# Optimization experiments

Measured on AMD Instinct MI355X. Metric: run time of the kernel, lower is better.

## Reference

```python
import jax, jax.numpy as jnp
import numpy as np

K = 3
K2 = K * K
EPS = 1e-5


def conv2d(x, w, stride=1, pad=1):
    return jax.lax.conv_general_dilated(
        x, w, (stride, stride), [(pad, pad), (pad, pad)],
        dimension_numbers=("NCHW", "OIHW", "NCHW"))


def bilinear_sample(x, py, px):
    """x: [B,C,H,W]; py,px: [B,Ho,Wo,K2] float sample coords.
    Zero padding outside bounds (torchvision deform_conv2d semantics).
    Returns [B,C,Ho,Wo,K2]."""
    B, C, H, W = x.shape
    Ho, Wo = py.shape[1], py.shape[2]
    y0 = jnp.floor(py)
    x0 = jnp.floor(px)
    wy1 = py - y0
    wx1 = px - x0
    x_flat = x.reshape(B, C, H * W)

    def gather(yi, xi):
        valid = (yi >= 0) & (yi < H) & (xi >= 0) & (xi < W)
        yc = jnp.clip(yi, 0, H - 1).astype(jnp.int32)
        xc = jnp.clip(xi, 0, W - 1).astype(jnp.int32)
        idx = (yc * W + xc).reshape(B, 1, -1)          # [B,1,N]
        v = jnp.take_along_axis(x_flat, idx, axis=2)   # [B,C,N]
        return v * valid.reshape(B, 1, -1).astype(x.dtype)

    w00 = ((1 - wy1) * (1 - wx1)).reshape(B, 1, -1)
    w01 = ((1 - wy1) * wx1).reshape(B, 1, -1)
    w10 = (wy1 * (1 - wx1)).reshape(B, 1, -1)
    w11 = (wy1 * wx1).reshape(B, 1, -1)
    val = (w00 * gather(y0, x0) + w01 * gather(y0, x0 + 1)
           + w10 * gather(y0 + 1, x0) + w11 * gather(y0 + 1, x0 + 1))
    return val.reshape(B, C, Ho, Wo, K2)


def deform_conv_bn_relu(x, d, offset_w, conv_w, gamma, beta):
    # offset branch: 3x3 conv on d, clamp to [-1,1]
    offset = jnp.clip(conv2d(d, offset_w, 1, 1), -1.0, 1.0)  # [B,2*K2,H,W]
    B, Cin, H, W = x.shape
    Cout = conv_w.shape[0]
    off = offset.reshape(B, K2, 2, H, W)
    dy = off[:, :, 0].transpose(0, 2, 3, 1)  # [B,H,W,K2]
    dx = off[:, :, 1].transpose(0, 2, 3, 1)
    kh = (jnp.arange(K2) // K).astype(jnp.float32)
    kw = (jnp.arange(K2) % K).astype(jnp.float32)
    # sample coords: out pixel + kernel tap - padding + learned offset
    py = (jnp.arange(H, dtype=jnp.float32)[None, :, None, None] - 1.0
          + kh[None, None, None, :] + dy)
    px = (jnp.arange(W, dtype=jnp.float32)[None, None, :, None] - 1.0
          + kw[None, None, None, :] + dx)
    sampled = bilinear_sample(x, py, px)  # [B,Cin,H,W,K2]
    out = jnp.einsum('bchwk,ock->bohw', sampled,
                     conv_w.reshape(Cout, Cin, K2))
    # BatchNorm2d (training forward: biased batch stats) + ReLU
    mean = out.mean(axis=(0, 2, 3))
    var = out.var(axis=(0, 2, 3))
    inv = gamma / jnp.sqrt(var + EPS)
    out = (out - mean[None, :, None, None]) * inv[None, :, None, None] \
        + beta[None, :, None, None]
    out = jax.nn.relu(out)
    return out, offset


def setup_inputs() -> dict:
    key = jax.random.key(0)
    k1, k2, k3, k4 = jax.random.split(key, 4)
    B, C, H, W = 4, 64, 160, 160
    Cout, offC = 64, 64
    x = jax.random.normal(k1, (B, C, H, W), dtype=jnp.float32)
    d = jax.random.normal(k2, (B, offC, H, W), dtype=jnp.float32)
    # torch zero-inits offset_conv; use small random weights so the
    # bilinear gather path is actually exercised with fractional offsets
    offset_w = jax.random.normal(k3, (2 * K2, offC, K, K), dtype=jnp.float32) * 0.01
    conv_w = jax.random.normal(k4, (Cout, C, K, K), dtype=jnp.float32) * (1.0 / np.sqrt(C * K2))
    gamma = jnp.ones((Cout,), dtype=jnp.float32)
    beta = jnp.zeros((Cout,), dtype=jnp.float32)
    return {"x": x, "d": d, "offset_w": offset_w, "conv_w": conv_w,
            "gamma": gamma, "beta": beta}


def reference(x, d, offset_w, conv_w, gamma, beta):
    return deform_conv_bn_relu(x, d, offset_w, conv_w, gamma, beta)
```

## Files before the change

### kernel.cpp

```cpp
#include <hip/hip_runtime.h>
#include <hip/hip_bf16.h>

#define BB 4
#define HH 160
#define WW 160
#define HWD (HH * WW)
#define OUT_ELEMS (BB * 64 * HWD)
#define OFF_ELEMS (BB * 18 * HWD)
#define EPSBN 1e-5f
#define CHSTRIDE (8 * HWD)
#define NSLOT 256

typedef __attribute__((ext_vector_type(8))) short bf16x8;
typedef __attribute__((ext_vector_type(4))) float f32x4;

__device__ inline unsigned pack2bf(float a, float b) {
  __hip_bfloat162 h2 = __float22bfloat162_rn(float2{a, b});
  unsigned u;
  __builtin_memcpy(&u, &h2, 4);
  return u;
}
__device__ inline unsigned short bf16bits(float a) {
  __hip_bfloat16 h = __float2bfloat16(a);
  unsigned short u;
  __builtin_memcpy(&u, &h, 2);
  return u;
}

__device__ inline void tile_map(int blk, int& b, int& ty0, int& tx0) {
  int t = (blk & 7) * 200 + (blk >> 3);
  b = t / 400;
  int r = t % 400;
  ty0 = (r / 10) * 4;
  tx0 = (r % 10) * 16;
}

__global__ void prep_kernel(const float* __restrict__ cw,
                            const float* __restrict__ ow,
                            unsigned short* __restrict__ Bp,
                            unsigned short* __restrict__ B2p,
                            float* __restrict__ part) {
  int i = blockIdx.x * 256 + threadIdx.x;
  if (i < 32768) part[i] = 0.f;
  if (i < 49152) {
    int j = i & 7, l = (i >> 3) & 63, rest = i >> 9;
    int ki = rest % 24, nt = rest / 24;
    int kp = ki * 32 + ((l >> 4) << 3) + j;
    int chunk = kp / 96, kq = kp % 96;
    int t = kq >> 3, c = kq & 7;
    int n = nt * 16 + (l & 15);
    float v = (t < 9) ? cw[n * 576 + (chunk * 8 + c) * 9 + t] : 0.f;
    Bp[i] = bf16bits(v);
  }
  if (i < 24576) {
    int j = i & 7, l = (i >> 3) & 63, rest = i >> 9;
    int ki = rest % 24, nt = rest / 24;
    int kp = ki * 32 + ((l >> 4) << 3) + j;
    int chunk = kp / 96, kq = kp % 96;
    int t = kq >> 3, c = kq & 7;
    int n = nt * 16 + (l & 15);
    float v = (t < 9 && n < 18) ? ow[n * 576 + (chunk * 8 + c) * 9 + t] : 0.f;
    B2p[i] = bf16bits(v);
  }
}

__global__ __launch_bounds__(256, 4) void fused_kernel(
    const float* __restrict__ x, const float* __restrict__ d,
    const bf16x8* __restrict__ Bp, const bf16x8* __restrict__ B2p,
    float* __restrict__ out, float* __restrict__ off_out,
    float* __restrict__ part) {
  int b, ty0, tx0;
  tile_map(blockIdx.x, b, ty0, tx0);
  const int tid = threadIdx.x;
  const int wv = tid >> 6, lane = tid & 63;
  const int lo = lane >> 4, li = lane & 15;
  const int px = li, py = wv;
  const int h = ty0 + py, w = tx0 + px;

  __shared__ float patch[189 * 12];
  __shared__ bf16x8 Af[768];
  __shared__ float offs_s[64 * 18];

  int goffx[6], laddrx[6];
  bool gokx[6];
#pragma unroll
  for (int i = 0; i < 6; ++i) {
    int l = tid + i * 256;
    int c = l / 189, rc = l % 189, r = rc / 21, col = rc % 21;
    int gy = ty0 - 2 + r, gx = tx0 - 2 + col;
    gokx[i] = (l < 1512) && gy >= 0 && gy < HH && gx >= 0 && gx < WW;
    goffx[i] = ((b * 64 + c) * HH + gy) * WW + gx;
    laddrx[i] = rc * 12 + c;
  }

  f32x4 acc0{0.f, 0.f, 0.f, 0.f}, acc1{0.f, 0.f, 0.f, 0.f};
  const int ntA = wv >> 1, mh = wv & 1;
  {
    int poff[3];
    bool tre[3];
#pragma unroll
    for (int kk = 0; kk < 3; ++kk) {
      int t = kk * 4 + lo;
      tre[kk] = (t < 9);
      poff[kk] = tre[kk] ? ((py + t / 3) * 18 + px + t % 3) : 0;
    }

    int goff[4], laddr[4];
    bool gok[4];
#pragma unroll
    for (int i = 0; i < 4; ++i) {
      int l = tid + i * 256;
      int c = l / 108, rc = l % 108, r = rc / 18, col = rc % 18;
      int gy = ty0 - 1 + r, gx = tx0 - 1 + col;
      gok[i] = (l < 864) && gy >= 0 && gy < HH && gx < WW && gx >= 0;
      goff[i] = ((b * 64 + c) * HH + gy) * WW + gx;
      laddr[i] = rc * 12 + c;
    }
    float g[4];
#pragma unroll
    for (int i = 0; i < 4; ++i) g[i] = gok[i] ? d[goff[i]] : 0.f;

    for (int chunk = 0; chunk < 8; ++chunk) {
      bf16x8 bw0 = B2p[((ntA * 24 + chunk * 3 + 0) << 6) + lane];
      bf16x8 bw1 = B2p[((ntA * 24 + chunk * 3 + 1) << 6) + lane];
      bf16x8 bw2 = B2p[((ntA * 24 + chunk * 3 + 2) << 6) + lane];
#pragma unroll
      for (int i = 0; i < 4; ++i) {
        int l = tid + i * 256;
        if (l < 864) patch[laddr[i]] = g[i];
      }
      __syncthreads();
      int nco = ((chunk < 7) ? (chunk + 1) : 7) * CHSTRIDE;
#pragma unroll
      for (int i = 0; i < 4; ++i) g[i] = gok[i] ? d[goff[i] + nco] : 0.f;
#pragma unroll
      for (int kk = 0; kk < 3; ++kk) {
        union { bf16x8 v; unsigned u[4]; } a;
        if (tre[kk]) {
          const float* q = patch + poff[kk] * 12;
          float4 c0 = *(const float4*)(q);
          float4 c1 = *(const float4*)(q + 4);
          a.u[0] = pack2bf(c0.x, c0.y);
          a.u[1] = pack2bf(c0.z, c0.w);
          a.u[2] = pack2bf(c1.x, c1.y);
          a.u[3] = pack2bf(c1.z, c1.w);
        } else {
          a.u[0] = a.u[1] = a.u[2] = a.u[3] = 0u;
        }
        Af[((wv * 3 + kk) << 6) + lane] = a.v;
      }
      __syncthreads();
#pragma unroll
      for (int kk = 0; kk < 3; ++kk) {
        bf16x8 bw = (kk == 0) ? bw0 : (kk == 1) ? bw1 : bw2;
        acc0 = __builtin_amdgcn_mfma_f32_16x16x32_bf16(
            Af[(((mh * 2) * 3 + kk) << 6) + lane], bw, acc0, 0, 0, 0);
        acc1 = __builtin_amdgcn_mfma_f32_16x16x32_bf16(
            Af[(((mh * 2 + 1) * 3 + kk) << 6) + lane], bw, acc1, 0, 0, 0);
      }
    }
  }

  float gv[6];
#pragma unroll
  for (int i = 0; i < 6; ++i) gv[i] = gokx[i] ? x[goffx[i]] : 0.f;

  {
    const int n = ntA * 16 + li;
    if (n < 18) {
#pragma unroll
      for (int f = 0; f < 2; ++f) {
        int mf = mh * 2 + f;
        f32x4 a = f ? acc1 : acc0;
        float* po =
            off_out + ((b * 18 + n) * HH + ty0 + mf) * WW + tx0 + lo * 4;
        float4 v;
        v.x = fminf(1.f, fmaxf(-1.f, a[0]));
        v.y = fminf(1.f, fmaxf(-1.f, a[1]));
        v.z = fminf(1.f, fmaxf(-1.f, a[2]));
        v.w = fminf(1.f, fmaxf(-1.f, a[3]));
        *(float4*)po = v;
        int pix = mf * 16 + lo * 4;
        offs_s[(pix + 0) * 18 + n] = v.x;
        offs_s[(pix + 1) * 18 + n] = v.y;
        offs_s[(pix + 2) * 18 + n] = v.z;
        offs_s[(pix + 3) * 18 + n] = v.w;
      }
    }
  }
  __syncthreads();

  int bs[3];
  float W00[3], W01[3], W10[3], W11[3];
  bool tre[3];
#pragma unroll
  for (int kk = 0; kk < 3; ++kk) {
    int t = kk * 4 + lo;
    tre[kk] = (t < 9);
    if (tre[kk]) {
      float dy = offs_s[(py * 16 + px) * 18 + 2 * t];
      float dx = offs_s[(py * 16 + px) * 18 + 2 * t + 1];
      float pyf = (float)(h - 1 + t / 3) + dy;
      float pxf = (float)(w - 1 + t % 3) + dx;
      float y0 = floorf(pyf), x0 = floorf(pxf);
      float wy = pyf - y0, wx = pxf - x0;
      bs[kk] = ((int)y0 - (ty0 - 2)) * 21 + ((int)x0 - (tx0 - 2));
      W00[kk] = (1.f - wy) * (1.f - wx);
      W01[kk] = (1.f - wy) * wx;
      W10[kk] = wy * (1.f - wx);
      W11[kk] = wy * wx;
    } else {
      bs[kk] = 0;
      W00[kk] = W01[kk] = W10[kk] = W11[kk] = 0.f;
    }
  }

  f32x4 acc[4];
#pragma unroll
  for (int i = 0; i < 4; ++i) acc[i] = f32x4{0.f, 0.f, 0.f, 0.f};
  const int nt = wv;

  for (int chunk = 0; chunk < 8; ++chunk) {
    bf16x8 bw0 = Bp[((nt * 24 + chunk * 3 + 0) << 6) + lane];
    bf16x8 bw1 = Bp[((nt * 24 + chunk * 3 + 1) << 6) + lane];
    bf16x8 bw2 = Bp[((nt * 24 + chunk * 3 + 2) << 6) + lane];
#pragma unroll
    for (int i = 0; i < 6; ++i) {
      int l = tid + i * 256;
      if (l < 1512) patch[laddrx[i]] = gv[i];
    }
    __syncthreads();
    int nco = ((chunk < 7) ? (chunk + 1) : 7) * CHSTRIDE;
#pragma unroll
    for (int i = 0; i < 6; ++i) gv[i] = gokx[i] ? x[goffx[i] + nco] : 0.f;
#pragma unroll
    for (int kk = 0; kk < 3; ++kk) {
      union { bf16x8 v; unsigned u[4]; } a;
      if (tre[kk]) {
        const float* q = patch + bs[kk] * 12;
        float4 p00a = *(const float4*)(q);
        float4 p00b = *(const float4*)(q + 4);
        float4 p01a = *(const float4*)(q + 12);
        float4 p01b = *(const float4*)(q + 16);
        float4 p10a = *(const float4*)(q + 252);
        float4 p10b = *(const float4*)(q + 256);
        float4 p11a = *(const float4*)(q + 264);
        float4 p11b = *(const float4*)(q + 268);
        float w0 = W00[kk], w1 = W01[kk], w2 = W10[kk], w3 = W11[kk];
        float v0 = fmaf(w3, p11a.x, fmaf(w2, p10a.x, fmaf(w1, p01a.x, w0 * p00a.x)));
        float v1 = fmaf(w3, p11a.y, fmaf(w2, p10a.y, fmaf(w1, p01a.y, w0 * p00a.y)));
        float v2 = fmaf(w3, p11a.z, fmaf(w2, p10a.z, fmaf(w1, p01a.z, w0 * p00a.z)));
        float v3 = fmaf(w3, p11a.w, fmaf(w2, p10a.w, fmaf(w1, p01a.w, w0 * p00a.w)));
        float v4 = fmaf(w3, p11b.x, fmaf(w2, p10b.x, fmaf(w1, p01b.x, w0 * p00b.x)));
        float v5 = fmaf(w3, p11b.y, fmaf(w2, p10b.y, fmaf(w1, p01b.y, w0 * p00b.y)));
        float v6 = fmaf(w3, p11b.z, fmaf(w2, p10b.z, fmaf(w1, p01b.z, w0 * p00b.z)));
        float v7 = fmaf(w3, p11b.w, fmaf(w2, p10b.w, fmaf(w1, p01b.w, w0 * p00b.w)));
        a.u[0] = pack2bf(v0, v1);
        a.u[1] = pack2bf(v2, v3);
        a.u[2] = pack2bf(v4, v5);
        a.u[3] = pack2bf(v6, v7);
      } else {
        a.u[0] = a.u[1] = a.u[2] = a.u[3] = 0u;
      }
      Af[((wv * 3 + kk) << 6) + lane] = a.v;
    }
    __syncthreads();
#pragma unroll
    for (int kk = 0; kk < 3; ++kk) {
      bf16x8 bw = (kk == 0) ? bw0 : (kk == 1) ? bw1 : bw2;
#pragma unroll
      for (int mf = 0; mf < 4; ++mf)
        acc[mf] = __builtin_amdgcn_mfma_f32_16x16x32_bf16(
            Af[((mf * 3 + kk) << 6) + lane], bw, acc[mf], 0, 0, 0);
    }
  }
  const int n = nt * 16 + li;
  float s = 0.f, s2 = 0.f;
#pragma unroll
  for (int mf = 0; mf < 4; ++mf) {
    float* po = out + ((b * 64 + n) * HH + ty0 + mf) * WW + tx0 + lo * 4;
    *(float4*)po = make_float4(acc[mf][0], acc[mf][1], acc[mf][2], acc[mf][3]);
#pragma unroll
    for (int r = 0; r < 4; ++r) {
      float v = acc[mf][r];
      s += v;
      s2 = fmaf(v, v, s2);
    }
  }
  s += __shfl_xor(s, 16);  s += __shfl_xor(s, 32);
  s2 += __shfl_xor(s2, 16); s2 += __shfl_xor(s2, 32);
  if (lo == 0) {
    int slot = blockIdx.x & (NSLOT - 1);
    atomicAdd(&part[n * NSLOT + slot], s);
    atomicAdd(&part[(64 + n) * NSLOT + slot], s2);
  }
}

__global__ __launch_bounds__(256) void reduce_kernel(
    const float* __restrict__ part, double* __restrict__ sums) {
  const int j = blockIdx.x;
  __shared__ double sh[256];
  sh[threadIdx.x] = (double)part[j * NSLOT + threadIdx.x];
  __syncthreads();
  for (int t = 128; t > 0; t >>= 1) {
    if (threadIdx.x < t) sh[threadIdx.x] += sh[threadIdx.x + t];
    __syncthreads();
  }
  if (threadIdx.x == 0) sums[j] = sh[0];
}

__global__ __launch_bounds__(256) void bnapply_kernel(
    float* __restrict__ out, const double* __restrict__ sums,
    const float* __restrict__ gamma, const float* __restrict__ beta) {
  const int i = blockIdx.x * 256 + threadIdx.x;
  if (i >= OUT_ELEMS / 4) return;
  const int o = (i / (HWD / 4)) & 63;
  const float n_inv = 1.0f / (float)(BB * HWD);
  float mean = (float)sums[o] * n_inv;
  float var = (float)sums[64 + o] * n_inv - mean * mean;
  float inv = gamma[o] * rsqrtf(var + EPSBN);
  float bt = beta[o];
  float4 v = ((float4*)out)[i];
  v.x = fmaxf(0.f, (v.x - mean) * inv + bt);
  v.y = fmaxf(0.f, (v.y - mean) * inv + bt);
  v.z = fmaxf(0.f, (v.z - mean) * inv + bt);
  v.w = fmaxf(0.f, (v.w - mean) * inv + bt);
  ((float4*)out)[i] = v;
}

extern "C" void kernel_launch(void* const* d_in, const int* in_sizes, int n_in,
                              void* d_out, int out_size, void* d_ws, size_t ws_size,
                              hipStream_t stream) {
  const float* x = (const float*)d_in[0];
  const float* d = (const float*)d_in[1];
  const float* ow = (const float*)d_in[2];
  const float* cw = (const float*)d_in[3];
  const float* gamma = (const float*)d_in[4];
  const float* beta = (const float*)d_in[5];

  float* out = (float*)d_out;
  float* off_out = out + OUT_ELEMS;

  double* sums = (double*)d_ws;
  unsigned short* Bp = (unsigned short*)((char*)d_ws + 1024);
  unsigned short* B2p = Bp + 49152;
  float* part = (float*)(B2p + 24576);

  prep_kernel<<<192, 256, 0, stream>>>(cw, ow, Bp, B2p, part);

  fused_kernel<<<1600, 256, 0, stream>>>(x, d, (const bf16x8*)Bp,
                                         (const bf16x8*)B2p, out, off_out,
                                         part);

  reduce_kernel<<<128, 256, 0, stream>>>(part, sums);
  bnapply_kernel<<<(OUT_ELEMS / 4 + 255) / 256, 256, 0, stream>>>(
      out, sums, gamma, beta);
}
```

Measured before the change: 161.7 us.

## Keep MFMA A-fragments in registers and double-buffer the input patch

Each wave now feeds its own sampled pixel-row fragments straight into MFMA as the A operand and loops over all output-channel tiles, so the Af shared-memory staging buffer and the second __syncthreads per channel chunk are gone. The input patch is double-buffered so the next chunk's store does not race with reads of the current one. In exchange each wave loads all the weight fragments per chunk, which raises register pressure and global/L2 weight traffic, and the epilogue now issues four times as many atomics per lane.

```diff
diff --git a/kernel.cpp b/kernel.cpp
--- a/kernel.cpp
+++ b/kernel.cpp
@@ -6,7 +6,6 @@
 #define WW 160
 #define HWD (HH * WW)
 #define OUT_ELEMS (BB * 64 * HWD)
-#define OFF_ELEMS (BB * 18 * HWD)
 #define EPSBN 1e-5f
 #define CHSTRIDE (8 * HWD)
 #define NSLOT 256
@@ -77,8 +76,7 @@
   const int px = li, py = wv;
   const int h = ty0 + py, w = tx0 + px;
 
-  __shared__ float patch[189 * 12];
-  __shared__ bf16x8 Af[768];
+  __shared__ float patch[2][189 * 12];
   __shared__ float offs_s[64 * 18];
 
   int goffx[6], laddrx[6];
@@ -93,16 +91,17 @@
     laddrx[i] = rc * 12 + c;
   }
 
-  f32x4 acc0{0.f, 0.f, 0.f, 0.f}, acc1{0.f, 0.f, 0.f, 0.f};
-  const int ntA = wv >> 1, mh = wv & 1;
+  int cur = 0;
+
+  f32x4 po0{0.f, 0.f, 0.f, 0.f}, po1{0.f, 0.f, 0.f, 0.f};
   {
     int poff[3];
-    bool tre[3];
+    bool tre1[3];
 #pragma unroll
     for (int kk = 0; kk < 3; ++kk) {
       int t = kk * 4 + lo;
-      tre[kk] = (t < 9);
-      poff[kk] = tre[kk] ? ((py + t / 3) * 18 + px + t % 3) : 0;
+      tre1[kk] = (t < 9);
+      poff[kk] = tre1[kk] ? ((py + t / 3) * 18 + px + t % 3) : 0;
     }
 
     int goff[4], laddr[4];
@@ -112,7 +111,7 @@
       int l = tid + i * 256;
       int c = l / 108, rc = l % 108, r = rc / 18, col = rc % 18;
       int gy = ty0 - 1 + r, gx = tx0 - 1 + col;
-      gok[i] = (l < 864) && gy >= 0 && gy < HH && gx < WW && gx >= 0;
+      gok[i] = (l < 864) && gy >= 0 && gy < HH && gx >= 0 && gx < WW;
       goff[i] = ((b * 64 + c) * HH + gy) * WW + gx;
       laddr[i] = rc * 12 + c;
     }
@@ -121,43 +120,40 @@
     for (int i = 0; i < 4; ++i) g[i] = gok[i] ? d[goff[i]] : 0.f;
 
     for (int chunk = 0; chunk < 8; ++chunk) {
-      bf16x8 bw0 = B2p[((ntA * 24 + chunk * 3 + 0) << 6) + lane];
-      bf16x8 bw1 = B2p[((ntA * 24 + chunk * 3 + 1) << 6) + lane];
-      bf16x8 bw2 = B2p[((ntA * 24 + chunk * 3 + 2) << 6) + lane];
 #pragma unroll
       for (int i = 0; i < 4; ++i) {
         int l = tid + i * 256;
-        if (l < 864) patch[laddr[i]] = g[i];
+        if (l < 864) patch[cur][laddr[i]] = g[i];
       }
       __syncthreads();
       int nco = ((chunk < 7) ? (chunk + 1) : 7) * CHSTRIDE;
 #pragma unroll
       for (int i = 0; i < 4; ++i) g[i] = gok[i] ? d[goff[i] + nco] : 0.f;
+      const bf16x8* Bc = B2p + ((chunk * 3) << 6) + lane;
+      bf16x8 w00 = Bc[0], w01 = Bc[64], w02 = Bc[128];
+      bf16x8 w10 = Bc[1536], w11 = Bc[1600], w12 = Bc[1664];
+      union { bf16x8 v; unsigned u[4]; } a[3];
 #pragma unroll
       for (int kk = 0; kk < 3; ++kk) {
-        union { bf16x8 v; unsigned u[4]; } a;
-        if (tre[kk]) {
-          const float* q = patch + poff[kk] * 12;
+        if (tre1[kk]) {
+          const float* q = patch[cur] + poff[kk] * 12;
           float4 c0 = *(const float4*)(q);
           float4 c1 = *(const float4*)(q + 4);
-          a.u[0] = pack2bf(c0.x, c0.y);
-          a.u[1] = pack2bf(c0.z, c0.w);
-          a.u[2] = pack2bf(c1.x, c1.y);
-          a.u[3] = pack2bf(c1.z, c1.w);
+          a[kk].u[0] = pack2bf(c0.x, c0.y);
+          a[kk].u[1] = pack2bf(c0.z, c0.w);
+          a[kk].u[2] = pack2bf(c1.x, c1.y);
+          a[kk].u[3] = pack2bf(c1.z, c1.w);
         } else {
-          a.u[0] = a.u[1] = a.u[2] = a.u[3] = 0u;
+          a[kk].u[0] = a[kk].u[1] = a[kk].u[2] = a[kk].u[3] = 0u;
         }
-        Af[((wv * 3 + kk) << 6) + lane] = a.v;
       }
-      __syncthreads();
-#pragma unroll
-      for (int kk = 0; kk < 3; ++kk) {
-        bf16x8 bw = (kk == 0) ? bw0 : (kk == 1) ? bw1 : bw2;
-        acc0 = __builtin_amdgcn_mfma_f32_16x16x32_bf16(
-            Af[(((mh * 2) * 3 + kk) << 6) + lane], bw, acc0, 0, 0, 0);
-        acc1 = __builtin_amdgcn_mfma_f32_16x16x32_bf16(
-            Af[(((mh * 2 + 1) * 3 + kk) << 6) + lane], bw, acc1, 0, 0, 0);
-      }
+      po0 = __builtin_amdgcn_mfma_f32_16x16x32_bf16(a[0].v, w00, po0, 0, 0, 0);
+      po0 = __builtin_amdgcn_mfma_f32_16x16x32_bf16(a[1].v, w01, po0, 0, 0, 0);
+      po0 = __builtin_amdgcn_mfma_f32_16x16x32_bf16(a[2].v, w02, po0, 0, 0, 0);
+      po1 = __builtin_amdgcn_mfma_f32_16x16x32_bf16(a[0].v, w10, po1, 0, 0, 0);
+      po1 = __builtin_amdgcn_mfma_f32_16x16x32_bf16(a[1].v, w11, po1, 0, 0, 0);
+      po1 = __builtin_amdgcn_mfma_f32_16x16x32_bf16(a[2].v, w12, po1, 0, 0, 0);
+      cur ^= 1;
     }
   }
 
@@ -166,21 +162,19 @@
   for (int i = 0; i < 6; ++i) gv[i] = gokx[i] ? x[goffx[i]] : 0.f;
 
   {
-    const int n = ntA * 16 + li;
-    if (n < 18) {
-#pragma unroll
-      for (int f = 0; f < 2; ++f) {
-        int mf = mh * 2 + f;
-        f32x4 a = f ? acc1 : acc0;
-        float* po =
-            off_out + ((b * 18 + n) * HH + ty0 + mf) * WW + tx0 + lo * 4;
+    const int y = ty0 + wv;
+#pragma unroll
+    for (int nf = 0; nf < 2; ++nf) {
+      int n = nf * 16 + li;
+      if (n < 18) {
+        f32x4 aa = nf ? po1 : po0;
         float4 v;
-        v.x = fminf(1.f, fmaxf(-1.f, a[0]));
-        v.y = fminf(1.f, fmaxf(-1.f, a[1]));
-        v.z = fminf(1.f, fmaxf(-1.f, a[2]));
-        v.w = fminf(1.f, fmaxf(-1.f, a[3]));
-        *(float4*)po = v;
-        int pix = mf * 16 + lo * 4;
+        v.x = fminf(1.f, fmaxf(-1.f, aa[0]));
+        v.y = fminf(1.f, fmaxf(-1.f, aa[1]));
+        v.z = fminf(1.f, fmaxf(-1.f, aa[2]));
+        v.w = fminf(1.f, fmaxf(-1.f, aa[3]));
+        *(float4*)(off_out + ((b * 18 + n) * HH + y) * WW + tx0 + lo * 4) = v;
+        int pix = wv * 16 + lo * 4;
         offs_s[(pix + 0) * 18 + n] = v.x;
         offs_s[(pix + 1) * 18 + n] = v.y;
         offs_s[(pix + 2) * 18 + n] = v.z;
@@ -198,10 +192,9 @@
     int t = kk * 4 + lo;
     tre[kk] = (t < 9);
     if (tre[kk]) {
-      float dy = offs_s[(py * 16 + px) * 18 + 2 * t];
-      float dx = offs_s[(py * 16 + px) * 18 + 2 * t + 1];
-      float pyf = (float)(h - 1 + t / 3) + dy;
-      float pxf = (float)(w - 1 + t % 3) + dx;
+      float2 dyx = *(const float2*)&offs_s[(wv * 16 + li) * 18 + 2 * t];
+      float pyf = (float)(h - 1 + t / 3) + dyx.x;
+      float pxf = (float)(w - 1 + t % 3) + dyx.y;
       float y0 = floorf(pyf), x0 = floorf(pxf);
       float wy = pyf - y0, wx = pxf - x0;
       bs[kk] = ((int)y0 - (ty0 - 2)) * 21 + ((int)x0 - (tx0 - 2));
@@ -218,26 +211,30 @@
   f32x4 acc[4];
 #pragma unroll
   for (int i = 0; i < 4; ++i) acc[i] = f32x4{0.f, 0.f, 0.f, 0.f};
-  const int nt = wv;
+  cur = 0;
 
   for (int chunk = 0; chunk < 8; ++chunk) {
-    bf16x8 bw0 = Bp[((nt * 24 + chunk * 3 + 0) << 6) + lane];
-    bf16x8 bw1 = Bp[((nt * 24 + chunk * 3 + 1) << 6) + lane];
-    bf16x8 bw2 = Bp[((nt * 24 + chunk * 3 + 2) << 6) + lane];
 #pragma unroll
     for (int i = 0; i < 6; ++i) {
       int l = tid + i * 256;
-      if (l < 1512) patch[laddrx[i]] = gv[i];
+      if (l < 1512) patch[cur][laddrx[i]] = gv[i];
     }
     __syncthreads();
     int nco = ((chunk < 7) ? (chunk + 1) : 7) * CHSTRIDE;
 #pragma unroll
     for (int i = 0; i < 6; ++i) gv[i] = gokx[i] ? x[goffx[i] + nco] : 0.f;
+    const bf16x8* Bc = Bp + ((chunk * 3) << 6) + lane;
+    bf16x8 bwf[4][3];
+#pragma unroll
+    for (int nf = 0; nf < 4; ++nf)
+#pragma unroll
+      for (int kk = 0; kk < 3; ++kk)
+        bwf[nf][kk] = Bc[(nf * 24 + kk) * 64];
+    union { bf16x8 v; unsigned u[4]; } a[3];
 #pragma unroll
     for (int kk = 0; kk < 3; ++kk) {
-      union { bf16x8 v; unsigned u[4]; } a;
       if (tre[kk]) {
-        const float* q = patch + bs[kk] * 12;
+        const float* q = patch[cur] + bs[kk] * 12;
         float4 p00a = *(const float4*)(q);
         float4 p00b = *(const float4*)(q + 4);
         float4 p01a = *(const float4*)(q + 12);
@@ -255,44 +252,52 @@
         float v5 = fmaf(w3, p11b.y, fmaf(w2, p10b.y, fmaf(w1, p01b.y, w0 * p00b.y)));
         float v6 = fmaf(w3, p11b.z, fmaf(w2, p10b.z, fmaf(w1, p01b.z, w0 * p00b.z)));
         float v7 = fmaf(w3, p11b.w, fmaf(w2, p10b.w, fmaf(w1, p01b.w, w0 * p00b.w)));
-        a.u[0] = pack2bf(v0, v1);
-        a.u[1] = pack2bf(v2, v3);
-        a.u[2] = pack2bf(v4, v5);
-        a.u[3] = pack2bf(v6, v7);
+        a[kk].u[0] = pack2bf(v0, v1);
+        a[kk].u[1] = pack2bf(v2, v3);
+        a[kk].u[2] = pack2bf(v4, v5);
+        a[kk].u[3] = pack2bf(v6, v7);
       } else {
-        a.u[0] = a.u[1] = a.u[2] = a.u[3] = 0u;
+        a[kk].u[0] = a[kk].u[1] = a[kk].u[2] = a[kk].u[3] = 0u;
       }
-      Af[((wv * 3 + kk) << 6) + lane] = a.v;
-    }
-    __syncthreads();
-#pragma unroll
-    for (int kk = 0; kk < 3; ++kk) {
-      bf16x8 bw = (kk == 0) ? bw0 : (kk == 1) ? bw1 : bw2;
-#pragma unroll
-      for (int mf = 0; mf < 4; ++mf)
-        acc[mf] = __builtin_amdgcn_mfma_f32_16x16x32_bf16(
-            Af[((mf * 3 + kk) << 6) + lane], bw, acc[mf], 0, 0, 0);
-    }
-  }
-  const int n = nt * 16 + li;
-  float s = 0.f, s2 = 0.f;
-#pragma unroll
-  for (int mf = 0; mf < 4; ++mf) {
-    float* po = out + ((b * 64 + n) * HH + ty0 + mf) * WW + tx0 + lo * 4;
-    *(float4*)po = make_float4(acc[mf][0], acc[mf][1], acc[mf][2], acc[mf][3]);
+    }
+#pragma unroll
+    for (int nf = 0; nf < 4; ++nf)
+#pragma unroll
+      for (int kk = 0; kk < 3; ++kk)
+        acc[nf] = __builtin_amdgcn_mfma_f32_16x16x32_bf16(
+            a[kk].v, bwf[nf][kk], acc[nf], 0, 0, 0);
+    cur ^= 1;
+  }
+
+  const int y = ty0 + wv;
+  float s[4], s2[4];
+#pragma unroll
+  for (int nf = 0; nf < 4; ++nf) {
+    s[nf] = 0.f;
+    s2[nf] = 0.f;
+    float* pout = out + ((b * 64 + nf * 16 + li) * HH + y) * WW + tx0 + lo * 4;
+    *(float4*)pout = make_float4(acc[nf][0], acc[nf][1], acc[nf][2], acc[nf][3]);
 #pragma unroll
     for (int r = 0; r < 4; ++r) {
-      float v = acc[mf][r];
-      s += v;
-      s2 = fmaf(v, v, s2);
-    }
-  }
-  s += __shfl_xor(s, 16);  s += __shfl_xor(s, 32);
-  s2 += __shfl_xor(s2, 16); s2 += __shfl_xor(s2, 32);
+      float v = acc[nf][r];
+      s[nf] += v;
+      s2[nf] = fmaf(v, v, s2[nf]);
+    }
+  }
+#pragma unroll
+  for (int nf = 0; nf < 4; ++nf) {
+    s[nf] += __shfl_xor(s[nf], 16);
+    s[nf] += __shfl_xor(s[nf], 32);
+    s2[nf] += __shfl_xor(s2[nf], 16);
+    s2[nf] += __shfl_xor(s2[nf], 32);
+  }
   if (lo == 0) {
     int slot = blockIdx.x & (NSLOT - 1);
-    atomicAdd(&part[n * NSLOT + slot], s);
-    atomicAdd(&part[(64 + n) * NSLOT + slot], s2);
+#pragma unroll
+    for (int nf = 0; nf < 4; ++nf) {
+      atomicAdd(&part[(nf * 16 + li) * NSLOT + slot], s[nf]);
+      atomicAdd(&part[(64 + nf * 16 + li) * NSLOT + slot], s2[nf]);
+    }
   }
 }
 
```

Result: slower. 480.4 us (+197.1%).

## Fuse BN stats reduction and apply into persistent kernel with grid barrier

Applied to the files above, without the earlier changes.

Turns the fused conv kernel into a persistent kernel of 800 blocks, each processing two tiles. A global atomic-counter grid barrier lets every block read the BN partial sums after all tiles finish, then apply BN+ReLU in place. The second tile's result stays in registers and is written once, while the first tile is written raw and re-read. This removes the separate reduce and bnapply launches and one full read/write pass over the output. The cost is a spin-wait barrier that assumes all 800 blocks are co-resident, so the kernel deadlocks if occupancy falls below 4 blocks per CU.

```diff
diff --git a/kernel.cpp b/kernel.cpp
--- a/kernel.cpp
+++ b/kernel.cpp
@@ -6,10 +6,10 @@
 #define WW 160
 #define HWD (HH * WW)
 #define OUT_ELEMS (BB * 64 * HWD)
-#define OFF_ELEMS (BB * 18 * HWD)
 #define EPSBN 1e-5f
 #define CHSTRIDE (8 * HWD)
-#define NSLOT 256
+#define NSLOT 128
+#define NBLK 800
 
 typedef __attribute__((ext_vector_type(8))) short bf16x8;
 typedef __attribute__((ext_vector_type(4))) float f32x4;
@@ -27,21 +27,15 @@
   return u;
 }
 
-__device__ inline void tile_map(int blk, int& b, int& ty0, int& tx0) {
-  int t = (blk & 7) * 200 + (blk >> 3);
-  b = t / 400;
-  int r = t % 400;
-  ty0 = (r / 10) * 4;
-  tx0 = (r % 10) * 16;
-}
-
 __global__ void prep_kernel(const float* __restrict__ cw,
                             const float* __restrict__ ow,
                             unsigned short* __restrict__ Bp,
                             unsigned short* __restrict__ B2p,
-                            float* __restrict__ part) {
+                            float* __restrict__ part,
+                            int* __restrict__ cnt) {
   int i = blockIdx.x * 256 + threadIdx.x;
-  if (i < 32768) part[i] = 0.f;
+  if (i == 0) *cnt = 0;
+  if (i < 16384) part[i] = 0.f;
   if (i < 49152) {
     int j = i & 7, l = (i >> 3) & 63, rest = i >> 9;
     int ki = rest % 24, nt = rest / 24;
@@ -64,86 +58,213 @@
   }
 }
 
-__global__ __launch_bounds__(256, 4) void fused_kernel(
+__global__ __launch_bounds__(256, 4) void persist_kernel(
     const float* __restrict__ x, const float* __restrict__ d,
     const bf16x8* __restrict__ Bp, const bf16x8* __restrict__ B2p,
     float* __restrict__ out, float* __restrict__ off_out,
-    float* __restrict__ part) {
-  int b, ty0, tx0;
-  tile_map(blockIdx.x, b, ty0, tx0);
+    float* __restrict__ part, int* __restrict__ cnt,
+    const float* __restrict__ gamma, const float* __restrict__ beta) {
   const int tid = threadIdx.x;
   const int wv = tid >> 6, lane = tid & 63;
   const int lo = lane >> 4, li = lane & 15;
   const int px = li, py = wv;
-  const int h = ty0 + py, w = tx0 + px;
 
   __shared__ float patch[189 * 12];
   __shared__ bf16x8 Af[768];
   __shared__ float offs_s[64 * 18];
 
-  int goffx[6], laddrx[6];
-  bool gokx[6];
-#pragma unroll
-  for (int i = 0; i < 6; ++i) {
-    int l = tid + i * 256;
-    int c = l / 189, rc = l % 189, r = rc / 21, col = rc % 21;
-    int gy = ty0 - 2 + r, gx = tx0 - 2 + col;
-    gokx[i] = (l < 1512) && gy >= 0 && gy < HH && gx >= 0 && gx < WW;
-    goffx[i] = ((b * 64 + c) * HH + gy) * WW + gx;
-    laddrx[i] = rc * 12 + c;
-  }
-
-  f32x4 acc0{0.f, 0.f, 0.f, 0.f}, acc1{0.f, 0.f, 0.f, 0.f};
-  const int ntA = wv >> 1, mh = wv & 1;
-  {
-    int poff[3];
+  f32x4 acc[4];
+  int b = 0, ty0 = 0, tx0 = 0;
+  int b1 = 0, ty1 = 0, tx1 = 0;
+
+  for (int j = 0; j < 2; ++j) {
+    __syncthreads();
+    {
+      int t = (blockIdx.x & 7) * 200 + (blockIdx.x >> 3) + j * 100;
+      b = t / 400;
+      int rr = t % 400;
+      ty0 = (rr / 10) * 4;
+      tx0 = (rr % 10) * 16;
+    }
+    const int h = ty0 + py, w = tx0 + px;
+
+    int goffx[6], laddrx[6];
+    bool gokx[6];
+#pragma unroll
+    for (int i = 0; i < 6; ++i) {
+      int l = tid + i * 256;
+      int c = l / 189, rc = l % 189, r = rc / 21, col = rc % 21;
+      int gy = ty0 - 2 + r, gx = tx0 - 2 + col;
+      gokx[i] = (l < 1512) && gy >= 0 && gy < HH && gx >= 0 && gx < WW;
+      goffx[i] = ((b * 64 + c) * HH + gy) * WW + gx;
+      laddrx[i] = rc * 12 + c;
+    }
+
+    f32x4 po0{0.f, 0.f, 0.f, 0.f}, po1{0.f, 0.f, 0.f, 0.f};
+    const int ntA = wv >> 1, mh = wv & 1;
+    {
+      int poff[3];
+      bool tre1[3];
+#pragma unroll
+      for (int kk = 0; kk < 3; ++kk) {
+        int t = kk * 4 + lo;
+        tre1[kk] = (t < 9);
+        poff[kk] = tre1[kk] ? ((py + t / 3) * 18 + px + t % 3) : 0;
+      }
+
+      int goff[4], laddr[4];
+      bool gok[4];
+#pragma unroll
+      for (int i = 0; i < 4; ++i) {
+        int l = tid + i * 256;
+        int c = l / 108, rc = l % 108, r = rc / 18, col = rc % 18;
+        int gy = ty0 - 1 + r, gx = tx0 - 1 + col;
+        gok[i] = (l < 864) && gy >= 0 && gy < HH && gx >= 0 && gx < WW;
+        goff[i] = ((b * 64 + c) * HH + gy) * WW + gx;
+        laddr[i] = rc * 12 + c;
+      }
+      float g[4];
+#pragma unroll
+      for (int i = 0; i < 4; ++i) g[i] = gok[i] ? d[goff[i]] : 0.f;
+
+      for (int chunk = 0; chunk < 8; ++chunk) {
+        bf16x8 bw0 = B2p[((ntA * 24 + chunk * 3 + 0) << 6) + lane];
+        bf16x8 bw1 = B2p[((ntA * 24 + chunk * 3 + 1) << 6) + lane];
+        bf16x8 bw2 = B2p[((ntA * 24 + chunk * 3 + 2) << 6) + lane];
+#pragma unroll
+        for (int i = 0; i < 4; ++i) {
+          int l = tid + i * 256;
+          if (l < 864) patch[laddr[i]] = g[i];
+        }
+        __syncthreads();
+        int nco = ((chunk < 7) ? (chunk + 1) : 7) * CHSTRIDE;
+#pragma unroll
+        for (int i = 0; i < 4; ++i) g[i] = gok[i] ? d[goff[i] + nco] : 0.f;
+#pragma unroll
+        for (int kk = 0; kk < 3; ++kk) {
+          union { bf16x8 v; unsigned u[4]; } a;
+          if (tre1[kk]) {
+            const float* q = patch + poff[kk] * 12;
+            float4 c0 = *(const float4*)(q);
+            float4 c1 = *(const float4*)(q + 4);
+            a.u[0] = pack2bf(c0.x, c0.y);
+            a.u[1] = pack2bf(c0.z, c0.w);
+            a.u[2] = pack2bf(c1.x, c1.y);
+            a.u[3] = pack2bf(c1.z, c1.w);
+          } else {
+            a.u[0] = a.u[1] = a.u[2] = a.u[3] = 0u;
+          }
+          Af[((wv * 3 + kk) << 6) + lane] = a.v;
+        }
+        __syncthreads();
+#pragma unroll
+        for (int kk = 0; kk < 3; ++kk) {
+          bf16x8 bw = (kk == 0) ? bw0 : (kk == 1) ? bw1 : bw2;
+          po0 = __builtin_amdgcn_mfma_f32_16x16x32_bf16(
+              Af[(((mh * 2) * 3 + kk) << 6) + lane], bw, po0, 0, 0, 0);
+          po1 = __builtin_amdgcn_mfma_f32_16x16x32_bf16(
+              Af[(((mh * 2 + 1) * 3 + kk) << 6) + lane], bw, po1, 0, 0, 0);
+        }
+      }
+    }
+
+    float gv[6];
+#pragma unroll
+    for (int i = 0; i < 6; ++i) gv[i] = gokx[i] ? x[goffx[i]] : 0.f;
+
+    {
+      const int n = ntA * 16 + li;
+      if (n < 18) {
+#pragma unroll
+        for (int f = 0; f < 2; ++f) {
+          int mf = mh * 2 + f;
+          f32x4 aa = f ? po1 : po0;
+          float* po =
+              off_out + ((b * 18 + n) * HH + ty0 + mf) * WW + tx0 + lo * 4;
+          float4 v;
+          v.x = fminf(1.f, fmaxf(-1.f, aa[0]));
+          v.y = fminf(1.f, fmaxf(-1.f, aa[1]));
+          v.z = fminf(1.f, fmaxf(-1.f, aa[2]));
+          v.w = fminf(1.f, fmaxf(-1.f, aa[3]));
+          *(float4*)po = v;
+          int pix = mf * 16 + lo * 4;
+          offs_s[(pix + 0) * 18 + n] = v.x;
+          offs_s[(pix + 1) * 18 + n] = v.y;
+          offs_s[(pix + 2) * 18 + n] = v.z;
+          offs_s[(pix + 3) * 18 + n] = v.w;
+        }
+      }
+    }
+    __syncthreads();
+
+    int bs[3];
+    float W00[3], W01[3], W10[3], W11[3];
     bool tre[3];
 #pragma unroll
     for (int kk = 0; kk < 3; ++kk) {
       int t = kk * 4 + lo;
       tre[kk] = (t < 9);
-      poff[kk] = tre[kk] ? ((py + t / 3) * 18 + px + t % 3) : 0;
-    }
-
-    int goff[4], laddr[4];
-    bool gok[4];
-#pragma unroll
-    for (int i = 0; i < 4; ++i) {
-      int l = tid + i * 256;
-      int c = l / 108, rc = l % 108, r = rc / 18, col = rc % 18;
-      int gy = ty0 - 1 + r, gx = tx0 - 1 + col;
-      gok[i] = (l < 864) && gy >= 0 && gy < HH && gx < WW && gx >= 0;
-      goff[i] = ((b * 64 + c) * HH + gy) * WW + gx;
-      laddr[i] = rc * 12 + c;
-    }
-    float g[4];
-#pragma unroll
-    for (int i = 0; i < 4; ++i) g[i] = gok[i] ? d[goff[i]] : 0.f;
+      if (tre[kk]) {
+        float dy = offs_s[(py * 16 + px) * 18 + 2 * t];
+        float dx = offs_s[(py * 16 + px) * 18 + 2 * t + 1];
+        float pyf = (float)(h - 1 + t / 3) + dy;
+        float pxf = (float)(w - 1 + t % 3) + dx;
+        float y0 = floorf(pyf), x0 = floorf(pxf);
+        float wy = pyf - y0, wx = pxf - x0;
+        bs[kk] = ((int)y0 - (ty0 - 2)) * 21 + ((int)x0 - (tx0 - 2));
+        W00[kk] = (1.f - wy) * (1.f - wx);
+        W01[kk] = (1.f - wy) * wx;
+        W10[kk] = wy * (1.f - wx);
+        W11[kk] = wy * wx;
+      } else {
+        bs[kk] = 0;
+        W00[kk] = W01[kk] = W10[kk] = W11[kk] = 0.f;
+      }
+    }
+
+#pragma unroll
+    for (int i = 0; i < 4; ++i) acc[i] = f32x4{0.f, 0.f, 0.f, 0.f};
+    const int nt = wv;
 
     for (int chunk = 0; chunk < 8; ++chunk) {
-      bf16x8 bw0 = B2p[((ntA * 24 + chunk * 3 + 0) << 6) + lane];
-      bf16x8 bw1 = B2p[((ntA * 24 + chunk * 3 + 1) << 6) + lane];
-      bf16x8 bw2 = B2p[((ntA * 24 + chunk * 3 + 2) << 6) + lane];
-#pragma unroll
-      for (int i = 0; i < 4; ++i) {
+      bf16x8 bw0 = Bp[((nt * 24 + chunk * 3 + 0) << 6) + lane];
+      bf16x8 bw1 = Bp[((nt * 24 + chunk * 3 + 1) << 6) + lane];
+      bf16x8 bw2 = Bp[((nt * 24 + chunk * 3 + 2) << 6) + lane];
+#pragma unroll
+      for (int i = 0; i < 6; ++i) {
         int l = tid + i * 256;
-        if (l < 864) patch[laddr[i]] = g[i];
+        if (l < 1512) patch[laddrx[i]] = gv[i];
       }
       __syncthreads();
       int nco = ((chunk < 7) ? (chunk + 1) : 7) * CHSTRIDE;
 #pragma unroll
-      for (int i = 0; i < 4; ++i) g[i] = gok[i] ? d[goff[i] + nco] : 0.f;
+      for (int i = 0; i < 6; ++i) gv[i] = gokx[i] ? x[goffx[i] + nco] : 0.f;
 #pragma unroll
       for (int kk = 0; kk < 3; ++kk) {
         union { bf16x8 v; unsigned u[4]; } a;
         if (tre[kk]) {
-          const float* q = patch + poff[kk] * 12;
-          float4 c0 = *(const float4*)(q);
-          float4 c1 = *(const float4*)(q + 4);
-          a.u[0] = pack2bf(c0.x, c0.y);
-          a.u[1] = pack2bf(c0.z, c0.w);
-          a.u[2] = pack2bf(c1.x, c1.y);
-          a.u[3] = pack2bf(c1.z, c1.w);
+          const float* q = patch + bs[kk] * 12;
+          float4 p00a = *(const float4*)(q);
+          float4 p00b = *(const float4*)(q + 4);
+          float4 p01a = *(const float4*)(q + 12);
+          float4 p01b = *(const float4*)(q + 16);
+          float4 p10a = *(const float4*)(q + 252);
+          float4 p10b = *(const float4*)(q + 256);
+          float4 p11a = *(const float4*)(q + 264);
+          float4 p11b = *(const float4*)(q + 268);
+          float w0 = W00[kk], w1 = W01[kk], w2 = W10[kk], w3 = W11[kk];
+          float v0 = fmaf(w3, p11a.x, fmaf(w2, p10a.x, fmaf(w1, p01a.x, w0 * p00a.x)));
+          float v1 = fmaf(w3, p11a.y, fmaf(w2, p10a.y, fmaf(w1, p01a.y, w0 * p00a.y)));
+          float v2 = fmaf(w3, p11a.z, fmaf(w2, p10a.z, fmaf(w1, p01a.z, w0 * p00a.z)));
+          float v3 = fmaf(w3, p11a.w, fmaf(w2, p10a.w, fmaf(w1, p01a.w, w0 * p00a.w)));
+          float v4 = fmaf(w3, p11b.x, fmaf(w2, p10b.x, fmaf(w1, p01b.x, w0 * p00b.x)));
+          float v5 = fmaf(w3, p11b.y, fmaf(w2, p10b.y, fmaf(w1, p01b.y, w0 * p00b.y)));
+          float v6 = fmaf(w3, p11b.z, fmaf(w2, p10b.z, fmaf(w1, p01b.z, w0 * p00b.z)));
+          float v7 = fmaf(w3, p11b.w, fmaf(w2, p10b.w, fmaf(w1, p01b.w, w0 * p00b.w)));
+          a.u[0] = pack2bf(v0, v1);
+          a.u[1] = pack2bf(v2, v3);
+          a.u[2] = pack2bf(v4, v5);
+          a.u[3] = pack2bf(v6, v7);
         } else {
           a.u[0] = a.u[1] = a.u[2] = a.u[3] = 0u;
         }
@@ -153,179 +274,86 @@
 #pragma unroll
       for (int kk = 0; kk < 3; ++kk) {
         bf16x8 bw = (kk == 0) ? bw0 : (kk == 1) ? bw1 : bw2;
-        acc0 = __builtin_amdgcn_mfma_f32_16x16x32_bf16(
-            Af[(((mh * 2) * 3 + kk) << 6) + lane], bw, acc0, 0, 0, 0);
-        acc1 = __builtin_amdgcn_mfma_f32_16x16x32_bf16(
-            Af[(((mh * 2 + 1) * 3 + kk) << 6) + lane], bw, acc1, 0, 0, 0);
-      }
-    }
-  }
-
-  float gv[6];
-#pragma unroll
-  for (int i = 0; i < 6; ++i) gv[i] = gokx[i] ? x[goffx[i]] : 0.f;
-
+#pragma unroll
+        for (int mf = 0; mf < 4; ++mf)
+          acc[mf] = __builtin_amdgcn_mfma_f32_16x16x32_bf16(
+              Af[((mf * 3 + kk) << 6) + lane], bw, acc[mf], 0, 0, 0);
+      }
+    }
+
+    const int n = nt * 16 + li;
+    float s = 0.f, s2 = 0.f;
+#pragma unroll
+    for (int mf = 0; mf < 4; ++mf) {
+      if (j == 0) {
+        float* po = out + ((b * 64 + n) * HH + ty0 + mf) * WW + tx0 + lo * 4;
+        *(float4*)po = make_float4(acc[mf][0], acc[mf][1], acc[mf][2], acc[mf][3]);
+      }
+#pragma unroll
+      for (int r = 0; r < 4; ++r) {
+        float v = acc[mf][r];
+        s += v;
+        s2 = fmaf(v, v, s2);
+      }
+    }
+    s += __shfl_xor(s, 16);  s += __shfl_xor(s, 32);
+    s2 += __shfl_xor(s2, 16); s2 += __shfl_xor(s2, 32);
+    if (lo == 0) {
+      int slot = blockIdx.x & (NSLOT - 1);
+      atomicAdd(&part[n * NSLOT + slot], s);
+      atomicAdd(&part[(64 + n) * NSLOT + slot], s2);
+    }
+    if (j == 0) { b1 = b; ty1 = ty0; tx1 = tx0; }
+  }
+
+  __syncthreads();
+  if (tid == 0) {
+    __threadfence();
+    atomicAdd(cnt, 1);
+    while (atomicAdd(cnt, 0) < NBLK) __builtin_amdgcn_s_sleep(32);
+  }
+  __syncthreads();
+
+  const int n = wv * 16 + li;
+  double s64 = 0.0, q64 = 0.0;
   {
-    const int n = ntA * 16 + li;
-    if (n < 18) {
-#pragma unroll
-      for (int f = 0; f < 2; ++f) {
-        int mf = mh * 2 + f;
-        f32x4 a = f ? acc1 : acc0;
-        float* po =
-            off_out + ((b * 18 + n) * HH + ty0 + mf) * WW + tx0 + lo * 4;
-        float4 v;
-        v.x = fminf(1.f, fmaxf(-1.f, a[0]));
-        v.y = fminf(1.f, fmaxf(-1.f, a[1]));
-        v.z = fminf(1.f, fmaxf(-1.f, a[2]));
-        v.w = fminf(1.f, fmaxf(-1.f, a[3]));
-        *(float4*)po = v;
-        int pix = mf * 16 + lo * 4;
-        offs_s[(pix + 0) * 18 + n] = v.x;
-        offs_s[(pix + 1) * 18 + n] = v.y;
-        offs_s[(pix + 2) * 18 + n] = v.z;
-        offs_s[(pix + 3) * 18 + n] = v.w;
-      }
-    }
-  }
-  __syncthreads();
-
-  int bs[3];
-  float W00[3], W01[3], W10[3], W11[3];
-  bool tre[3];
-#pragma unroll
-  for (int kk = 0; kk < 3; ++kk) {
-    int t = kk * 4 + lo;
-    tre[kk] = (t < 9);
-    if (tre[kk]) {
-      float dy = offs_s[(py * 16 + px) * 18 + 2 * t];
-      float dx = offs_s[(py * 16 + px) * 18 + 2 * t + 1];
-      float pyf = (float)(h - 1 + t / 3) + dy;
-      float pxf = (float)(w - 1 + t % 3) + dx;
-      float y0 = floorf(pyf), x0 = floorf(pxf);
-      float wy = pyf - y0, wx = pxf - x0;
-      bs[kk] = ((int)y0 - (ty0 - 2)) * 21 + ((int)x0 - (tx0 - 2));
-      W00[kk] = (1.f - wy) * (1.f - wx);
-      W01[kk] = (1.f - wy) * wx;
-      W10[kk] = wy * (1.f - wx);
-      W11[kk] = wy * wx;
-    } else {
-      bs[kk] = 0;
-      W00[kk] = W01[kk] = W10[kk] = W11[kk] = 0.f;
-    }
-  }
-
-  f32x4 acc[4];
-#pragma unroll
-  for (int i = 0; i < 4; ++i) acc[i] = f32x4{0.f, 0.f, 0.f, 0.f};
-  const int nt = wv;
-
-  for (int chunk = 0; chunk < 8; ++chunk) {
-    bf16x8 bw0 = Bp[((nt * 24 + chunk * 3 + 0) << 6) + lane];
-    bf16x8 bw1 = Bp[((nt * 24 + chunk * 3 + 1) << 6) + lane];
-    bf16x8 bw2 = Bp[((nt * 24 + chunk * 3 + 2) << 6) + lane];
-#pragma unroll
-    for (int i = 0; i < 6; ++i) {
-      int l = tid + i * 256;
-      if (l < 1512) patch[laddrx[i]] = gv[i];
-    }
-    __syncthreads();
-    int nco = ((chunk < 7) ? (chunk + 1) : 7) * CHSTRIDE;
-#pragma unroll
-    for (int i = 0; i < 6; ++i) gv[i] = gokx[i] ? x[goffx[i] + nco] : 0.f;
-#pragma unroll
-    for (int kk = 0; kk < 3; ++kk) {
-      union { bf16x8 v; unsigned u[4]; } a;
-      if (tre[kk]) {
-        const float* q = patch + bs[kk] * 12;
-        float4 p00a = *(const float4*)(q);
-        float4 p00b = *(const float4*)(q + 4);
-        float4 p01a = *(const float4*)(q + 12);
-        float4 p01b = *(const float4*)(q + 16);
-        float4 p10a = *(const float4*)(q + 252);
-        float4 p10b = *(const float4*)(q + 256);
-        float4 p11a = *(const float4*)(q + 264);
-        float4 p11b = *(const float4*)(q + 268);
-        float w0 = W00[kk], w1 = W01[kk], w2 = W10[kk], w3 = W11[kk];
-        float v0 = fmaf(w3, p11a.x, fmaf(w2, p10a.x, fmaf(w1, p01a.x, w0 * p00a.x)));
-        float v1 = fmaf(w3, p11a.y, fmaf(w2, p10a.y, fmaf(w1, p01a.y, w0 * p00a.y)));
-        float v2 = fmaf(w3, p11a.z, fmaf(w2, p10a.z, fmaf(w1, p01a.z, w0 * p00a.z)));
-        float v3 = fmaf(w3, p11a.w, fmaf(w2, p10a.w, fmaf(w1, p01a.w, w0 * p00a.w)));
-        float v4 = fmaf(w3, p11b.x, fmaf(w2, p10b.x, fmaf(w1, p01b.x, w0 * p00b.x)));
-        float v5 = fmaf(w3, p11b.y, fmaf(w2, p10b.y, fmaf(w1, p01b.y, w0 * p00b.y)));
-        float v6 = fmaf(w3, p11b.z, fmaf(w2, p10b.z, fmaf(w1, p01b.z, w0 * p00b.z)));
-        float v7 = fmaf(w3, p11b.w, fmaf(w2, p10b.w, fmaf(w1, p01b.w, w0 * p00b.w)));
-        a.u[0] = pack2bf(v0, v1);
-        a.u[1] = pack2bf(v2, v3);
-        a.u[2] = pack2bf(v4, v5);
-        a.u[3] = pack2bf(v6, v7);
-      } else {
-        a.u[0] = a.u[1] = a.u[2] = a.u[3] = 0u;
-      }
-      Af[((wv * 3 + kk) << 6) + lane] = a.v;
-    }
-    __syncthreads();
-#pragma unroll
-    for (int kk = 0; kk < 3; ++kk) {
-      bf16x8 bw = (kk == 0) ? bw0 : (kk == 1) ? bw1 : bw2;
-#pragma unroll
-      for (int mf = 0; mf < 4; ++mf)
-        acc[mf] = __builtin_amdgcn_mfma_f32_16x16x32_bf16(
-            Af[((mf * 3 + kk) << 6) + lane], bw, acc[mf], 0, 0, 0);
-    }
-  }
-  const int n = nt * 16 + li;
-  float s = 0.f, s2 = 0.f;
+    const float* pr = part + n * NSLOT + lo * 32;
+    const float* qr = part + (64 + n) * NSLOT + lo * 32;
+#pragma unroll
+    for (int k = 0; k < 8; ++k) {
+      float4 a4 = *(const float4*)(pr + k * 4);
+      float4 c4 = *(const float4*)(qr + k * 4);
+      s64 += (double)a4.x + (double)a4.y + (double)a4.z + (double)a4.w;
+      q64 += (double)c4.x + (double)c4.y + (double)c4.z + (double)c4.w;
+    }
+  }
+  s64 += __shfl_xor(s64, 16); s64 += __shfl_xor(s64, 32);
+  q64 += __shfl_xor(q64, 16); q64 += __shfl_xor(q64, 32);
+  const float n_inv = 1.0f / (float)(BB * HWD);
+  const float mean = (float)s64 * n_inv;
+  const float var = (float)q64 * n_inv - mean * mean;
+  const float bninv = gamma[n] * rsqrtf(var + EPSBN);
+  const float bnbt = beta[n];
+
 #pragma unroll
   for (int mf = 0; mf < 4; ++mf) {
-    float* po = out + ((b * 64 + n) * HH + ty0 + mf) * WW + tx0 + lo * 4;
-    *(float4*)po = make_float4(acc[mf][0], acc[mf][1], acc[mf][2], acc[mf][3]);
-#pragma unroll
-    for (int r = 0; r < 4; ++r) {
-      float v = acc[mf][r];
-      s += v;
-      s2 = fmaf(v, v, s2);
-    }
-  }
-  s += __shfl_xor(s, 16);  s += __shfl_xor(s, 32);
-  s2 += __shfl_xor(s2, 16); s2 += __shfl_xor(s2, 32);
-  if (lo == 0) {
-    int slot = blockIdx.x & (NSLOT - 1);
-    atomicAdd(&part[n * NSLOT + slot], s);
-    atomicAdd(&part[(64 + n) * NSLOT + slot], s2);
-  }
-}
-
-__global__ __launch_bounds__(256) void reduce_kernel(
-    const float* __restrict__ part, double* __restrict__ sums) {
-  const int j = blockIdx.x;
-  __shared__ double sh[256];
-  sh[threadIdx.x] = (double)part[j * NSLOT + threadIdx.x];
-  __syncthreads();
-  for (int t = 128; t > 0; t >>= 1) {
-    if (threadIdx.x < t) sh[threadIdx.x] += sh[threadIdx.x + t];
-    __syncthreads();
-  }
-  if (threadIdx.x == 0) sums[j] = sh[0];
-}
-
-__global__ __launch_bounds__(256) void bnapply_kernel(
-    float* __restrict__ out, const double* __restrict__ sums,
-    const float* __restrict__ gamma, const float* __restrict__ beta) {
-  const int i = blockIdx.x * 256 + threadIdx.x;
-  if (i >= OUT_ELEMS / 4) return;
-  const int o = (i / (HWD / 4)) & 63;
-  const float n_inv = 1.0f / (float)(BB * HWD);
-  float mean = (float)sums[o] * n_inv;
-  float var = (float)sums[64 + o] * n_inv - mean * mean;
-  float inv = gamma[o] * rsqrtf(var + EPSBN);
-  float bt = beta[o];
-  float4 v = ((float4*)out)[i];
-  v.x = fmaxf(0.f, (v.x - mean) * inv + bt);
-  v.y = fmaxf(0.f, (v.y - mean) * inv + bt);
-  v.z = fmaxf(0.f, (v.z - mean) * inv + bt);
-  v.w = fmaxf(0.f, (v.w - mean) * inv + bt);
-  ((float4*)out)[i] = v;
+    float4 v;
+    v.x = fmaxf(0.f, (acc[mf][0] - mean) * bninv + bnbt);
+    v.y = fmaxf(0.f, (acc[mf][1] - mean) * bninv + bnbt);
+    v.z = fmaxf(0.f, (acc[mf][2] - mean) * bninv + bnbt);
+    v.w = fmaxf(0.f, (acc[mf][3] - mean) * bninv + bnbt);
+    *(float4*)(out + ((b * 64 + n) * HH + ty0 + mf) * WW + tx0 + lo * 4) = v;
+  }
+#pragma unroll
+  for (int mf = 0; mf < 4; ++mf) {
+    float* po = out + ((b1 * 64 + n) * HH + ty1 + mf) * WW + tx1 + lo * 4;
+    float4 v = *(float4*)po;
+    v.x = fmaxf(0.f, (v.x - mean) * bninv + bnbt);
+    v.y = fmaxf(0.f, (v.y - mean) * bninv + bnbt);
+    v.z = fmaxf(0.f, (v.z - mean) * bninv + bnbt);
+    v.w = fmaxf(0.f, (v.w - mean) * bninv + bnbt);
+    *(float4*)po = v;
+  }
 }
 
 extern "C" void kernel_launch(void* const* d_in, const int* in_sizes, int n_in,
@@ -341,18 +369,14 @@
   float* out = (float*)d_out;
   float* off_out = out + OUT_ELEMS;
 
-  double* sums = (double*)d_ws;
   unsigned short* Bp = (unsigned short*)((char*)d_ws + 1024);
   unsigned short* B2p = Bp + 49152;
   float* part = (float*)(B2p + 24576);
-
-  prep_kernel<<<192, 256, 0, stream>>>(cw, ow, Bp, B2p, part);
-
-  fused_kernel<<<1600, 256, 0, stream>>>(x, d, (const bf16x8*)Bp,
-                                         (const bf16x8*)B2p, out, off_out,
-                                         part);
-
-  reduce_kernel<<<128, 256, 0, stream>>>(part, sums);
-  bnapply_kernel<<<(OUT_ELEMS / 4 + 255) / 256, 256, 0, stream>>>(
-      out, sums, gamma, beta);
-}
+  int* cnt = (int*)(part + 16384);
+
+  prep_kernel<<<192, 256, 0, stream>>>(cw, ow, Bp, B2p, part, cnt);
+
+  persist_kernel<<<NBLK, 256, 0, stream>>>(x, d, (const bf16x8*)Bp,
+                                           (const bf16x8*)B2p, out, off_out,
+                                           part, cnt, gamma, beta);
+}
```

New measurement: 308.7 us. 90.9% more time.
